# Kernel tuning notes

Hardware: AMD Instinct MI355X
Metric: run time of the kernel (lower is better)

The kernel has to match this reference:

```python
import jax, jax.numpy as jnp
import numpy as np

KH, KW, STRIDE = 5, 5, 1
OUT_CH = 64


def setup_inputs() -> dict:
    key = jax.random.key(0)
    k1, k2 = jax.random.split(key)
    x = jax.random.normal(k1, (16, 1, 256, 256), dtype=jnp.float32)
    # kaiming_uniform_(a=sqrt(5)) on fan_in=25 gives bound ~= sqrt(6/((1+5)*25)) ~= 0.2
    w = jax.random.uniform(k2, (OUT_CH, 1, KH, KW), dtype=jnp.float32, minval=-0.2, maxval=0.2)
    w = w.at[0].set(0.0)  # reset_parameters zeroes the first filter
    return {"x": x, "weight": w}


def reference(x, weight):
    """Faithful vectorized RBF_Conv2d forward.

    Original: for each output pixel (k,l), cdist between the flattened window
    (B, kh*kw) and flattened weights (O, kh*kw), std = sample std (ddof=1) of
    the (B,O) distance matrix, output = gauss(dist, std) = exp(-0.5*(d/std)^2).
    """
    B = x.shape[0]
    O = weight.shape[0]
    # im2col: (B, P=kh*kw, Ho, Wo), valid padding (in_channels == 1)
    patches = jax.lax.conv_general_dilated_patches(
        x, (KH, KW), (STRIDE, STRIDE), 'VALID')
    wf = weight.reshape(O, -1)                                  # (O, P)
    pn = jnp.sum(patches * patches, axis=1)                     # (B, Ho, Wo)
    wn = jnp.sum(wf * wf, axis=1)                               # (O,)
    cross = jnp.einsum('bphw,op->bohw', patches, wf)            # (B, O, Ho, Wo)
    d2 = pn[:, None] + wn[None, :, None, None] - 2.0 * cross
    dist = jnp.sqrt(jnp.maximum(d2, 1e-12))                     # euclidean cdist
    # per-output-pixel sample std (ddof=1) over the (B, O) distance matrix
    mean = jnp.mean(dist, axis=(0, 1), keepdims=True)           # (1,1,Ho,Wo)
    var = jnp.sum((dist - mean) ** 2, axis=(0, 1), keepdims=True) / (B * O - 1)
    std = jnp.sqrt(var)
    # gauss RBF
    return jnp.exp(-0.5 * (dist / std) ** 2)
```

## Files before the change

kernel.cpp:

```cpp
#include <hip/hip_runtime.h>

typedef float v2f __attribute__((ext_vector_type(2)));

#define KH 5
#define KW 5
#define HH 256
#define WW 256
#define HO 252
#define WO 252
#define NB 16
#define NO 64
#define PLANE (HO * WO)
#define TLW 64
#define XCOLS (TLW + KW - 1)

__global__ __launch_bounds__(512, 4)
void rbf_conv2d_kernel(const float* __restrict__ x, const float* __restrict__ w,
                       float* __restrict__ out) {
    __shared__ float xs[NB][KH][XCOLS];
    __shared__ float wn[NO];
    __shared__ float pS1[8][TLW];
    __shared__ float pS2[8][TLW];
    __shared__ float cinv_s[TLW];

    const int t = threadIdx.x;
    const int k = blockIdx.y;
    const int a = (4 * k) & 15;
    const int l0 = a - TLW + TLW * (int)blockIdx.x;
    if (l0 >= WO || l0 + TLW <= 0) return;

    for (int idx = t; idx < NB * KH * XCOLS; idx += 512) {
        int b   = idx / (KH * XCOLS);
        int rem = idx - b * (KH * XCOLS);
        int r   = rem / XCOLS;
        int c   = rem - r * XCOLS;
        int col = l0 + c;
        col = col < 0 ? 0 : (col > WW - 1 ? WW - 1 : col);
        xs[b][r][c] = x[(b * HH + k + r) * WW + col];
    }
    if (t < NO) {
        float s = 0.f;
        #pragma unroll
        for (int i = 0; i < 25; ++i) { float v = w[t * 25 + i]; s = fmaf(v, v, s); }
        wn[t] = s;
    }
    __syncthreads();

    const int lane = t & 63;
    const int bg   = __builtin_amdgcn_readfirstlane(t >> 6);
    const int l    = l0 + lane;

    float s1 = 0.f, s2 = 0.f;
    #pragma unroll 1
    for (int bi = 0; bi < 2; ++bi) {
        const int b = bg + 8 * bi;
        float pr[25];
        float pn = 0.f;
        #pragma unroll
        for (int r = 0; r < KH; ++r)
            #pragma unroll
            for (int c = 0; c < KW; ++c) {
                float v = xs[b][r][lane + c];
                pr[r * KW + c] = v;
                pn = fmaf(v, v, pn);
            }
        v2f prv[12];
        #pragma unroll
        for (int i = 0; i < 12; ++i) { prv[i].x = pr[2 * i]; prv[i].y = pr[2 * i + 1]; }
        const float pr24 = pr[24];

        #pragma unroll 8
        for (int j = 0; j < 32; ++j) {
            float cr0, cr1;
            {
                const float* __restrict__ wr = w + (2 * j) * 25;
                v2f acc = {0.f, 0.f};
                #pragma unroll
                for (int i = 0; i < 12; ++i) {
                    v2f wv_; wv_.x = wr[2 * i]; wv_.y = wr[2 * i + 1];
                    acc = __builtin_elementwise_fma(prv[i], wv_, acc);
                }
                cr0 = acc.x + acc.y + pr24 * wr[24];
            }
            {
                const float* __restrict__ wr = w + (2 * j + 1) * 25;
                v2f acc = {0.f, 0.f};
                #pragma unroll
                for (int i = 0; i < 12; ++i) {
                    v2f wv_; wv_.x = wr[2 * i]; wv_.y = wr[2 * i + 1];
                    acc = __builtin_elementwise_fma(prv[i], wv_, acc);
                }
                cr1 = acc.x + acc.y + pr24 * wr[24];
            }
            v2f wn2 = *(const v2f*)&wn[2 * j];
            float d20 = fmaxf(fmaf(-2.f, cr0, pn + wn2.x), 1e-12f);
            float d21 = fmaxf(fmaf(-2.f, cr1, pn + wn2.y), 1e-12f);
            s2 += d20 + d21;
            s1 += __builtin_amdgcn_sqrtf(d20) + __builtin_amdgcn_sqrtf(d21);
        }
    }
    pS1[bg][lane] = s1;
    pS2[bg][lane] = s2;
    __syncthreads();

    if (t < TLW) {
        float S1 = 0.f, S2 = 0.f;
        #pragma unroll
        for (int q = 0; q < 8; ++q) { S1 += pS1[q][t]; S2 += pS2[q][t]; }
        const float var = (S2 - S1 * S1 * (1.0f / 1024.0f)) * (1.0f / 1023.0f);
        cinv_s[t] = -0.72134752044448170368f / var;
    }
    __syncthreads();

    const float ci  = cinv_s[lane];
    const bool  ok  = ((unsigned)l < (unsigned)WO);
    #pragma unroll 1
    for (int bi = 0; bi < 2; ++bi) {
        const int b = bg + 8 * bi;
        float pr[25];
        float pn = 0.f;
        #pragma unroll
        for (int r = 0; r < KH; ++r)
            #pragma unroll
            for (int c = 0; c < KW; ++c) {
                float v = xs[b][r][lane + c];
                pr[r * KW + c] = v;
                pn = fmaf(v, v, pn);
            }
        v2f prv[12];
        #pragma unroll
        for (int i = 0; i < 12; ++i) { prv[i].x = pr[2 * i]; prv[i].y = pr[2 * i + 1]; }
        const float pr24 = pr[24];

        const int base_b = (b * NO) * PLANE + k * WO + l;
        #pragma unroll 8
        for (int j = 0; j < 32; ++j) {
            float cr0, cr1;
            {
                const float* __restrict__ wr = w + (2 * j) * 25;
                v2f acc = {0.f, 0.f};
                #pragma unroll
                for (int i = 0; i < 12; ++i) {
                    v2f wv_; wv_.x = wr[2 * i]; wv_.y = wr[2 * i + 1];
                    acc = __builtin_elementwise_fma(prv[i], wv_, acc);
                }
                cr0 = acc.x + acc.y + pr24 * wr[24];
            }
            {
                const float* __restrict__ wr = w + (2 * j + 1) * 25;
                v2f acc = {0.f, 0.f};
                #pragma unroll
                for (int i = 0; i < 12; ++i) {
                    v2f wv_; wv_.x = wr[2 * i]; wv_.y = wr[2 * i + 1];
                    acc = __builtin_elementwise_fma(prv[i], wv_, acc);
                }
                cr1 = acc.x + acc.y + pr24 * wr[24];
            }
            v2f wn2 = *(const v2f*)&wn[2 * j];
            float d20 = fmaxf(fmaf(-2.f, cr0, pn + wn2.x), 1e-12f);
            float d21 = fmaxf(fmaf(-2.f, cr1, pn + wn2.y), 1e-12f);
            float e0 = exp2f(d20 * ci);
            float e1 = exp2f(d21 * ci);
            if (ok) {
                out[base_b + (2 * j) * PLANE]     = e0;
                out[base_b + (2 * j + 1) * PLANE] = e1;
            }
        }
    }
}

extern "C" void kernel_launch(void* const* d_in, const int* in_sizes, int n_in,
                              void* d_out, int out_size, void* d_ws, size_t ws_size,
                              hipStream_t stream) {
    const float* x = (const float*)d_in[0];
    const float* w = (const float*)d_in[1];
    float* out = (float*)d_out;
    dim3 grid(5, HO);
    rbf_conv2d_kernel<<<grid, 512, 0, stream>>>(x, w, out);
}
```

Measured before the change: 340.2 us.

## Split into stats kernel and per-(batch,filter) output kernel with workspace buffers

Splits the fused kernel into two. A stats kernel computes the per-pixel inverse variance and stores patch norms in workspace. An output kernel tiled by (row chunk, filter, batch) then recomputes the 25-tap correlation with that filter's weights held in registers, and writes 8 contiguous outputs per thread as vec4 stores. This replaces the strided per-channel scalar stores and the redundant second pass over all 64 filters, at the cost of a second launch and extra workspace traffic for pn and cinv.

New measurement: 333.2 us. -2.1%, faster.

```diff
diff --git a/kernel.cpp b/kernel.cpp
--- a/kernel.cpp
+++ b/kernel.cpp
@@ -1,6 +1,7 @@
 #include <hip/hip_runtime.h>
 
 typedef float v2f __attribute__((ext_vector_type(2)));
+typedef float v4f __attribute__((ext_vector_type(4)));
 
 #define KH 5
 #define KW 5
@@ -11,31 +12,32 @@
 #define NB 16
 #define NO 64
 #define PLANE (HO * WO)
-#define TLW 64
-#define XCOLS (TLW + KW - 1)
+
+#define CINV_FLOATS 63616
+#define PN_FLOATS   (NB * PLANE + 64)
+
+#define T1W 64
+#define XC1 69
 
 __global__ __launch_bounds__(512, 4)
-void rbf_conv2d_kernel(const float* __restrict__ x, const float* __restrict__ w,
-                       float* __restrict__ out) {
-    __shared__ float xs[NB][KH][XCOLS];
+void rbf_stats_kernel(const float* __restrict__ x, const float* __restrict__ w,
+                      float* __restrict__ cinvb, float* __restrict__ pnb) {
+    __shared__ float xs[NB][KH][XC1];
     __shared__ float wn[NO];
-    __shared__ float pS1[8][TLW];
-    __shared__ float pS2[8][TLW];
-    __shared__ float cinv_s[TLW];
-
-    const int t = threadIdx.x;
-    const int k = blockIdx.y;
-    const int a = (4 * k) & 15;
-    const int l0 = a - TLW + TLW * (int)blockIdx.x;
-    if (l0 >= WO || l0 + TLW <= 0) return;
-
-    for (int idx = t; idx < NB * KH * XCOLS; idx += 512) {
-        int b   = idx / (KH * XCOLS);
-        int rem = idx - b * (KH * XCOLS);
-        int r   = rem / XCOLS;
-        int c   = rem - r * XCOLS;
+    __shared__ float pS1[8][T1W];
+    __shared__ float pS2[8][T1W];
+
+    const int t  = threadIdx.x;
+    const int k  = blockIdx.y;
+    const int l0 = (int)blockIdx.x * T1W;
+
+    for (int idx = t; idx < NB * KH * 68; idx += 512) {
+        int b   = idx / (KH * 68);
+        int rem = idx - b * (KH * 68);
+        int r   = rem / 68;
+        int c   = rem - r * 68;
         int col = l0 + c;
-        col = col < 0 ? 0 : (col > WW - 1 ? WW - 1 : col);
+        col = col > WW - 1 ? WW - 1 : col;
         xs[b][r][c] = x[(b * HH + k + r) * WW + col];
     }
     if (t < NO) {
@@ -64,6 +66,8 @@
                 pr[r * KW + c] = v;
                 pn = fmaf(v, v, pn);
             }
+        if (l < WO) pnb[b * PLANE + k * WO + l] = pn;
+
         v2f prv[12];
         #pragma unroll
         for (int i = 0; i < 12; ++i) { prv[i].x = pr[2 * i]; prv[i].y = pr[2 * i + 1]; }
@@ -103,69 +107,91 @@
     pS2[bg][lane] = s2;
     __syncthreads();
 
-    if (t < TLW) {
+    if (t < T1W) {
         float S1 = 0.f, S2 = 0.f;
         #pragma unroll
         for (int q = 0; q < 8; ++q) { S1 += pS1[q][t]; S2 += pS2[q][t]; }
         const float var = (S2 - S1 * S1 * (1.0f / 1024.0f)) * (1.0f / 1023.0f);
-        cinv_s[t] = -0.72134752044448170368f / var;
-    }
+        const int ll = l0 + t;
+        if (ll < WO) cinvb[k * WO + ll] = -0.72134752044448170368f / var;
+    }
+}
+
+#define RCH 42
+#define XR  46
+#define XW  264
+
+__global__ __launch_bounds__(512, 4)
+void rbf_out_kernel(const float* __restrict__ x, const float* __restrict__ w,
+                    const float* __restrict__ cinvb, const float* __restrict__ pnb,
+                    float* __restrict__ out) {
+    __shared__ float xs[XR][XW];
+
+    const int t  = threadIdx.x;
+    const int k0 = (int)blockIdx.x * RCH;
+    const int o  = blockIdx.y;
+    const int b  = blockIdx.z;
+
+    for (int idx = t; idx < XR * 64; idx += 512) {
+        const int row = idx >> 6, c4 = (idx & 63) << 2;
+        *(v4f*)&xs[row][c4] = *(const v4f*)&x[(b * HH + k0 + row) * WW + c4];
+    }
+    if (t < XR * 2) {
+        const int row = t >> 1, c = 256 + ((t & 1) << 2);
+        v4f z = {0.f, 0.f, 0.f, 0.f};
+        *(v4f*)&xs[row][c] = z;
+    }
+    const float* __restrict__ wp = w + o * 25;
+    float ws[25]; float wnv = 0.f;
+    #pragma unroll
+    for (int i = 0; i < 25; ++i) { ws[i] = wp[i]; wnv = fmaf(ws[i], ws[i], wnv); }
     __syncthreads();
 
-    const float ci  = cinv_s[lane];
-    const bool  ok  = ((unsigned)l < (unsigned)WO);
+    const int ct = t & 31;
+    const int rs = t >> 5;
+    const int c0 = ct << 3;
+    const int obase = (b * NO + o) * PLANE;
+
     #pragma unroll 1
-    for (int bi = 0; bi < 2; ++bi) {
-        const int b = bg + 8 * bi;
-        float pr[25];
-        float pn = 0.f;
-        #pragma unroll
-        for (int r = 0; r < KH; ++r)
+    for (int it = 0; it < 3; ++it) {
+        const int ki = it * 16 + rs;
+        if (ki >= RCH) continue;
+        const int gk = k0 + ki;
+
+        float cr[8] = {0.f, 0.f, 0.f, 0.f, 0.f, 0.f, 0.f, 0.f};
+        #pragma unroll
+        for (int r = 0; r < KH; ++r) {
+            const float* rowp = &xs[ki + r][c0];
+            v4f va = *(const v4f*)rowp;
+            v4f vb = *(const v4f*)(rowp + 4);
+            v4f vc = *(const v4f*)(rowp + 8);
+            float v[12] = {va.x, va.y, va.z, va.w, vb.x, vb.y, vb.z, vb.w,
+                           vc.x, vc.y, vc.z, vc.w};
             #pragma unroll
-            for (int c = 0; c < KW; ++c) {
-                float v = xs[b][r][lane + c];
-                pr[r * KW + c] = v;
-                pn = fmaf(v, v, pn);
-            }
-        v2f prv[12];
-        #pragma unroll
-        for (int i = 0; i < 12; ++i) { prv[i].x = pr[2 * i]; prv[i].y = pr[2 * i + 1]; }
-        const float pr24 = pr[24];
-
-        const int base_b = (b * NO) * PLANE + k * WO + l;
-        #pragma unroll 8
-        for (int j = 0; j < 32; ++j) {
-            float cr0, cr1;
-            {
-                const float* __restrict__ wr = w + (2 * j) * 25;
-                v2f acc = {0.f, 0.f};
+            for (int j = 0; j < 8; ++j)
                 #pragma unroll
-                for (int i = 0; i < 12; ++i) {
-                    v2f wv_; wv_.x = wr[2 * i]; wv_.y = wr[2 * i + 1];
-                    acc = __builtin_elementwise_fma(prv[i], wv_, acc);
-                }
-                cr0 = acc.x + acc.y + pr24 * wr[24];
-            }
-            {
-                const float* __restrict__ wr = w + (2 * j + 1) * 25;
-                v2f acc = {0.f, 0.f};
-                #pragma unroll
-                for (int i = 0; i < 12; ++i) {
-                    v2f wv_; wv_.x = wr[2 * i]; wv_.y = wr[2 * i + 1];
-                    acc = __builtin_elementwise_fma(prv[i], wv_, acc);
-                }
-                cr1 = acc.x + acc.y + pr24 * wr[24];
-            }
-            v2f wn2 = *(const v2f*)&wn[2 * j];
-            float d20 = fmaxf(fmaf(-2.f, cr0, pn + wn2.x), 1e-12f);
-            float d21 = fmaxf(fmaf(-2.f, cr1, pn + wn2.y), 1e-12f);
-            float e0 = exp2f(d20 * ci);
-            float e1 = exp2f(d21 * ci);
-            if (ok) {
-                out[base_b + (2 * j) * PLANE]     = e0;
-                out[base_b + (2 * j + 1) * PLANE] = e1;
-            }
+                for (int c = 0; c < KW; ++c)
+                    cr[j] = fmaf(v[j + c], ws[r * KW + c], cr[j]);
         }
+
+        const int px = gk * WO + c0;
+        v4f pA = *(const v4f*)&pnb[b * PLANE + px];
+        v4f pB = *(const v4f*)&pnb[b * PLANE + px + 4];
+        v4f cA = *(const v4f*)&cinvb[px];
+        v4f cB = *(const v4f*)&cinvb[px + 4];
+
+        v4f oA, oB;
+        oA.x = exp2f(fmaxf(fmaf(-2.f, cr[0], pA.x + wnv), 1e-12f) * cA.x);
+        oA.y = exp2f(fmaxf(fmaf(-2.f, cr[1], pA.y + wnv), 1e-12f) * cA.y);
+        oA.z = exp2f(fmaxf(fmaf(-2.f, cr[2], pA.z + wnv), 1e-12f) * cA.z);
+        oA.w = exp2f(fmaxf(fmaf(-2.f, cr[3], pA.w + wnv), 1e-12f) * cA.w);
+        oB.x = exp2f(fmaxf(fmaf(-2.f, cr[4], pB.x + wnv), 1e-12f) * cB.x);
+        oB.y = exp2f(fmaxf(fmaf(-2.f, cr[5], pB.y + wnv), 1e-12f) * cB.y);
+        oB.z = exp2f(fmaxf(fmaf(-2.f, cr[6], pB.z + wnv), 1e-12f) * cB.z);
+        oB.w = exp2f(fmaxf(fmaf(-2.f, cr[7], pB.w + wnv), 1e-12f) * cB.w);
+
+        *(v4f*)&out[obase + px] = oA;
+        if (ct < 31) *(v4f*)&out[obase + px + 4] = oB;
     }
 }
 
@@ -174,7 +200,12 @@
                               hipStream_t stream) {
     const float* x = (const float*)d_in[0];
     const float* w = (const float*)d_in[1];
-    float* out = (float*)d_out;
-    dim3 grid(5, HO);
-    rbf_conv2d_kernel<<<grid, 512, 0, stream>>>(x, w, out);
+    float* out  = (float*)d_out;
+    float* cinv = (float*)d_ws;
+    float* pnb  = (float*)d_ws + CINV_FLOATS;
+
+    dim3 g1(4, HO);
+    rbf_stats_kernel<<<g1, 512, 0, stream>>>(x, w, cinv, pnb);
+    dim3 g2(6, NO, NB);
+    rbf_out_kernel<<<g2, 512, 0, stream>>>(x, w, cinv, pnb, out);
 }
```
